# Performance work log

Measured on AMD Instinct MI355X. Metric: run time of the kernel, lower is better.

The kernel has to match this reference:

```python
import jax, jax.numpy as jnp
import numpy as np

B, S, D = 4, 2048, 1024


def setup_inputs() -> dict:
    key = jax.random.key(0)
    ks = jax.random.split(key, 4)
    scale = 1.0 / np.sqrt(D)
    x = jax.random.normal(ks[0], (B, S, D), dtype=jnp.float32)
    Wk = jax.random.normal(ks[1], (D, D), dtype=jnp.float32) * scale
    Wq = jax.random.normal(ks[2], (D, D), dtype=jnp.float32) * scale
    Wv = jax.random.normal(ks[3], (D, D), dtype=jnp.float32) * scale
    bk = jnp.zeros((D,), dtype=jnp.float32)
    bq = jnp.zeros((D,), dtype=jnp.float32)
    bv = jnp.zeros((D,), dtype=jnp.float32)
    return {"x": x, "Wk": Wk, "bk": bk, "Wq": Wq, "bq": bq,
            "Wv": Wv, "bv": bv, "dims": 2}


def correlated_weight(k, q, v, dims):
    # correlation between every query position and every key position,
    # scaled by sqrt(d) for numerical stability (standard correlation attn)
    d = q.shape[-1]
    scores = jnp.einsum("bqd,bkd->bqk", q, k) / jnp.sqrt(jnp.asarray(d, q.dtype))
    w = jax.nn.softmax(scores, axis=dims)          # [B, S, S]
    return jnp.einsum("bqk,bkd->bqd", w, v)        # [B, S, D]


def reference(x, Wk, bk, Wq, bq, Wv, bv, dims):
    # injected key/query/value funcs instantiated as Linear layers
    k = jnp.einsum("bsd,de->bse", x, Wk) + bk
    q = jnp.einsum("bsd,de->bse", x, Wq) + bq
    v = jnp.einsum("bsd,de->bse", x, Wv) + bv
    return correlated_weight(k, q, v, dims)
```

## Files before the change

### kernel.cpp

```cpp
#include <hip/hip_runtime.h>
#include <hip/hip_bf16.h>
#include <stdint.h>


typedef unsigned short u16;
typedef __bf16 bf16x8 __attribute__((ext_vector_type(8)));
typedef float  f32x4  __attribute__((ext_vector_type(4)));
typedef u16    u16x4  __attribute__((ext_vector_type(4)));
typedef u16    u16x8  __attribute__((ext_vector_type(8)));

__device__ __forceinline__ u16 f2bf(float f) {
  union { float f; uint32_t u; } v; v.f = f;
  uint32_t r = v.u + 0x7fffu + ((v.u >> 16) & 1u);
  return (u16)(r >> 16);
}
__device__ __forceinline__ float bf2f(u16 b) {
  union { uint32_t u; float f; } v; v.u = (uint32_t)b << 16; return v.f;
}

#define GLD_LDS16(gp, lp) __builtin_amdgcn_global_load_lds(                   \
    (const __attribute__((address_space(1))) void*)(gp),                      \
    (__attribute__((address_space(3))) void*)(lp), 16, 0, 0)


__global__ __launch_bounds__(256) void conv_x(const float* __restrict__ in,
                                              u16* __restrict__ out, int n) {
  int i = (blockIdx.x * 256 + threadIdx.x) * 4;
  if (i >= n) return;
  float4 v = *(const float4*)(in + i);
  u16x4 o; o.x = f2bf(v.x); o.y = f2bf(v.y); o.z = f2bf(v.z); o.w = f2bf(v.w);
  *(u16x4*)(out + i) = o;
}

__global__ __launch_bounds__(256) void trans_conv_w3(const float* __restrict__ Wq,
                                                     const float* __restrict__ Wk,
                                                     const float* __restrict__ Wv,
                                                     u16* __restrict__ Wt) {
  __shared__ float t[32][33];
  const float* W = blockIdx.z == 0 ? Wq : (blockIdx.z == 1 ? Wk : Wv);
  u16* dst = Wt + (size_t)blockIdx.z * 1024 * 1024;
  int e0 = blockIdx.x * 32, d0 = blockIdx.y * 32;
  #pragma unroll
  for (int i = 0; i < 4; ++i)
    t[threadIdx.y + i * 8][threadIdx.x] =
        W[(size_t)(d0 + threadIdx.y + i * 8) * 1024 + e0 + threadIdx.x];
  __syncthreads();
  #pragma unroll
  for (int i = 0; i < 4; ++i)
    dst[(size_t)(e0 + threadIdx.y + i * 8) * 1024 + d0 + threadIdx.x] =
        f2bf(t[threadIdx.x][threadIdx.y + i * 8]);
}

__global__ __launch_bounds__(256) void concat_bias(const float* __restrict__ bq,
                                                   const float* __restrict__ bk,
                                                   const float* __restrict__ bv,
                                                   float* __restrict__ bc) {
  int i = blockIdx.x * 256 + threadIdx.x;
  if (i >= 3072) return;
  bc[i] = (i < 1024) ? bq[i] : (i < 2048 ? bk[i - 1024] : bv[i - 2048]);
}

__global__ __launch_bounds__(256) void trans_v(const u16* __restrict__ qkv,
                                               u16* __restrict__ vT) {
  __shared__ u16 t[64][72];
  int b = blockIdx.z;
  int s0 = blockIdx.x * 64, e0 = blockIdx.y * 64;
  const u16* src = qkv + (size_t)b * 2048 * 3072 + 2048;
  u16* dst = vT + (size_t)b * 1024 * 2048;
  int tx = threadIdx.x & 7, ty = threadIdx.x >> 3;
  #pragma unroll
  for (int rr = 0; rr < 64; rr += 32)
    *(u16x8*)&t[ty + rr][tx * 8] =
        *(const u16x8*)(src + (size_t)(s0 + ty + rr) * 3072 + e0 + tx * 8);
  __syncthreads();
  #pragma unroll
  for (int rr = 0; rr < 64; rr += 32) {
    int er = ty + rr;
    u16x8 o;
    #pragma unroll
    for (int j = 0; j < 8; ++j) o[j] = t[tx * 8 + j][er];
    *(u16x8*)(dst + (size_t)(e0 + er) * 2048 + s0 + tx * 8) = o;
  }
}


template <int BN, bool OUT_BF16, bool BIAS, bool EXP, bool DIV>
__global__ __launch_bounds__(256)
void gemm16(const u16* __restrict__ A, int lda, long long sA,
            const u16* __restrict__ B, int ldb, long long sB,
            void* __restrict__ C, int ldc, long long sC,
            const float* __restrict__ aux, int K, float scale) {
  constexpr int NJ = BN / 32;
  __shared__ u16 As[128 * 64];
  __shared__ u16 Bs[BN * 64];
  const int lane = threadIdx.x & 63;
  const int wv = threadIdx.x >> 6;

  const u16* Ab = A + (size_t)blockIdx.z * sA + (size_t)blockIdx.y * 128 * lda;
  const u16* Bb = B + (size_t)blockIdx.z * sB + (size_t)blockIdx.x * BN * ldb;

  const int srow = lane >> 3;
  const int scol = ((lane & 7) ^ (lane >> 3)) * 8;
  const int row16 = lane & 15;
  const int quad = lane >> 4;
  const int rx = lane & 7;
  const int wm = (wv >> 1) * 64;
  const int wn = (wv & 1) * (BN / 2);

  f32x4 acc[4][NJ];
  #pragma unroll
  for (int i = 0; i < 4; ++i)
    #pragma unroll
    for (int j = 0; j < NJ; ++j) acc[i][j] = (f32x4)0.0f;

  for (int k0 = 0; k0 < K; k0 += 64) {
    #pragma unroll
    for (int i = 0; i < 4; ++i) {
      int r = wv * 32 + i * 8;
      GLD_LDS16(Ab + (size_t)(r + srow) * lda + k0 + scol, As + r * 64);
    }
    #pragma unroll
    for (int i = 0; i < BN / 32; ++i) {
      int r = wv * (BN / 4) + i * 8;
      GLD_LDS16(Bb + (size_t)(r + srow) * ldb + k0 + scol, Bs + r * 64);
    }
    __syncthreads();

    bf16x8 af[4][2], bfr[NJ][2];
    #pragma unroll
    for (int t = 0; t < 2; ++t) {
      int pc = ((t * 4 + quad) ^ rx) * 8;
      #pragma unroll
      for (int i = 0; i < 4; ++i)
        af[i][t] = *(const bf16x8*)(As + (wm + i * 16 + row16) * 64 + pc);
      #pragma unroll
      for (int j = 0; j < NJ; ++j)
        bfr[j][t] = *(const bf16x8*)(Bs + (wn + j * 16 + row16) * 64 + pc);
    }
    #pragma unroll
    for (int i = 0; i < 4; ++i)
      #pragma unroll
      for (int j = 0; j < NJ; ++j)
        #pragma unroll
        for (int t = 0; t < 2; ++t)
          acc[i][j] = __builtin_amdgcn_mfma_f32_16x16x32_bf16(
              af[i][t], bfr[j][t], acc[i][j], 0, 0, 0);
    __syncthreads();
  }

  const int crow0 = blockIdx.y * 128 + wm + quad * 4;
  const int ccol0 = blockIdx.x * BN + wn + row16;
  u16* Cb = (u16*)C + (size_t)blockIdx.z * sC;
  float* Cf = (float*)C + (size_t)blockIdx.z * sC;
  float rl[4][4];
  if (DIV) {
    const float* lz = aux + (size_t)blockIdx.z * 2048;
    #pragma unroll
    for (int i = 0; i < 4; ++i)
      #pragma unroll
      for (int r = 0; r < 4; ++r)
        rl[i][r] = 1.0f / lz[blockIdx.y * 128 + wm + quad * 4 + i * 16 + r];
  }
  #pragma unroll
  for (int i = 0; i < 4; ++i) {
    #pragma unroll
    for (int r = 0; r < 4; ++r) {
      int m = crow0 + i * 16 + r;
      #pragma unroll
      for (int j = 0; j < NJ; ++j) {
        int n = ccol0 + j * 16;
        float v = acc[i][j][r] * scale;
        if (BIAS) v += aux[n];
        if (EXP) v = exp2f(v);
        if (DIV) v *= rl[i][r];
        if (OUT_BF16) Cb[(size_t)m * ldc + n] = f2bf(v);
        else          Cf[(size_t)m * ldc + n] = v;
      }
    }
  }
}


__global__ __launch_bounds__(256) void rowsum(const u16* __restrict__ P,
                                              float* __restrict__ l) {
  const int lane = threadIdx.x & 63;
  const int row = blockIdx.x * 4 + (threadIdx.x >> 6);
  const u16* r = P + (size_t)row * 2048;
  float s = 0.f;
  #pragma unroll
  for (int c = 0; c < 4; ++c) {
    u16x8 w = *(const u16x8*)(r + c * 512 + lane * 8);
    #pragma unroll
    for (int j = 0; j < 8; ++j) s += bf2f(w[j]);
  }
  #pragma unroll
  for (int off = 32; off > 0; off >>= 1) s += __shfl_down(s, off);
  if (lane == 0) l[row] = s;
}


extern "C" void kernel_launch(void* const* d_in, const int* in_sizes, int n_in,
                              void* d_out, int out_size, void* d_ws, size_t ws_size,
                              hipStream_t stream) {
  const float* x  = (const float*)d_in[0];
  const float* Wk = (const float*)d_in[1];
  const float* bk = (const float*)d_in[2];
  const float* Wq = (const float*)d_in[3];
  const float* bq = (const float*)d_in[4];
  const float* Wv = (const float*)d_in[5];
  const float* bv = (const float*)d_in[6];
  float* out = (float*)d_out;

  char* ws = (char*)d_ws;
  u16*   xb  = (u16*)(ws + 0);
  u16*   wt  = (u16*)(ws + 16777216);
  float* bc  = (float*)(ws + 23068672);
  u16*   qkv = (u16*)(ws + 23080960);
  u16*   vT  = (u16*)(ws + 73412608);
  u16*   P   = (u16*)(ws + 90189824);
  float* l   = (float*)(ws + 123744256);
  (void)in_sizes; (void)n_in; (void)out_size; (void)ws_size;

  conv_x<<<8192, 256, 0, stream>>>(x, xb, 8388608);
  trans_conv_w3<<<dim3(32, 32, 3), dim3(32, 8), 0, stream>>>(Wq, Wk, Wv, wt);
  concat_bias<<<12, 256, 0, stream>>>(bq, bk, bv, bc);

  gemm16<128, true, true, false, false><<<dim3(24, 64, 1), 256, 0, stream>>>(
      xb, 1024, 0LL, wt, 1024, 0LL, (void*)qkv, 3072, 0LL, bc, 1024, 1.0f);

  trans_v<<<dim3(32, 16, 4), 256, 0, stream>>>(qkv, vT);

  gemm16<128, true, false, true, false><<<dim3(16, 16, 4), 256, 0, stream>>>(
      qkv, 3072, 2048LL * 3072, qkv + 1024, 3072, 2048LL * 3072,
      (void*)P, 2048, 2048LL * 2048, nullptr, 1024, 0.03125f * 1.44269504f);

  rowsum<<<2048, 256, 0, stream>>>(P, l);

  gemm16<64, false, false, false, true><<<dim3(16, 16, 4), 256, 0, stream>>>(
      P, 2048, 2048LL * 2048, vT, 2048, 1024LL * 2048,
      out, 1024, 2048LL * 1024, l, 2048, 1.0f);
}
```

Measured before the change: 290.9 us.

## Use 32x32 MFMA, fuse rowsum into exp GEMM via atomics, merge prep kernels

Switches the GEMM inner product from 16x16x32 to 32x32x16 bf16 MFMA tiles, which changes the fragment loads and the epilogue index mapping. The separate rowsum pass is removed: the score GEMM now sums its exp values per row with shuffles and adds them atomically into l. The three input-prep kernels plus the zeroing of l are merged into one launch. This drops a full read of P and two kernel launches, at the cost of atomics and a summation order that is no longer deterministic. The row sums now use the fp32 exp values rather than the rounded bf16 P entries.

```diff
diff --git a/kernel.cpp b/kernel.cpp
--- a/kernel.cpp
+++ b/kernel.cpp
@@ -5,7 +5,7 @@
 
 typedef unsigned short u16;
 typedef __bf16 bf16x8 __attribute__((ext_vector_type(8)));
-typedef float  f32x4  __attribute__((ext_vector_type(4)));
+typedef float  f32x16 __attribute__((ext_vector_type(16)));
 typedef u16    u16x4  __attribute__((ext_vector_type(4)));
 typedef u16    u16x8  __attribute__((ext_vector_type(8)));
 
@@ -14,50 +14,53 @@
   uint32_t r = v.u + 0x7fffu + ((v.u >> 16) & 1u);
   return (u16)(r >> 16);
 }
-__device__ __forceinline__ float bf2f(u16 b) {
-  union { uint32_t u; float f; } v; v.u = (uint32_t)b << 16; return v.f;
-}
 
 #define GLD_LDS16(gp, lp) __builtin_amdgcn_global_load_lds(                   \
     (const __attribute__((address_space(1))) void*)(gp),                      \
     (__attribute__((address_space(3))) void*)(lp), 16, 0, 0)
 
 
-__global__ __launch_bounds__(256) void conv_x(const float* __restrict__ in,
-                                              u16* __restrict__ out, int n) {
-  int i = (blockIdx.x * 256 + threadIdx.x) * 4;
-  if (i >= n) return;
-  float4 v = *(const float4*)(in + i);
-  u16x4 o; o.x = f2bf(v.x); o.y = f2bf(v.y); o.z = f2bf(v.z); o.w = f2bf(v.w);
-  *(u16x4*)(out + i) = o;
-}
-
-__global__ __launch_bounds__(256) void trans_conv_w3(const float* __restrict__ Wq,
-                                                     const float* __restrict__ Wk,
-                                                     const float* __restrict__ Wv,
-                                                     u16* __restrict__ Wt) {
+__global__ __launch_bounds__(256) void prep(const float* __restrict__ x,
+                                            const float* __restrict__ Wq,
+                                            const float* __restrict__ Wk,
+                                            const float* __restrict__ Wv,
+                                            const float* __restrict__ bq,
+                                            const float* __restrict__ bk,
+                                            const float* __restrict__ bv,
+                                            u16* __restrict__ xb,
+                                            u16* __restrict__ wt,
+                                            float* __restrict__ bc,
+                                            float* __restrict__ l) {
   __shared__ float t[32][33];
-  const float* W = blockIdx.z == 0 ? Wq : (blockIdx.z == 1 ? Wk : Wv);
-  u16* dst = Wt + (size_t)blockIdx.z * 1024 * 1024;
-  int e0 = blockIdx.x * 32, d0 = blockIdx.y * 32;
-  #pragma unroll
-  for (int i = 0; i < 4; ++i)
-    t[threadIdx.y + i * 8][threadIdx.x] =
-        W[(size_t)(d0 + threadIdx.y + i * 8) * 1024 + e0 + threadIdx.x];
-  __syncthreads();
-  #pragma unroll
-  for (int i = 0; i < 4; ++i)
-    dst[(size_t)(e0 + threadIdx.y + i * 8) * 1024 + d0 + threadIdx.x] =
-        f2bf(t[threadIdx.x][threadIdx.y + i * 8]);
-}
-
-__global__ __launch_bounds__(256) void concat_bias(const float* __restrict__ bq,
-                                                   const float* __restrict__ bk,
-                                                   const float* __restrict__ bv,
-                                                   float* __restrict__ bc) {
-  int i = blockIdx.x * 256 + threadIdx.x;
-  if (i >= 3072) return;
-  bc[i] = (i < 1024) ? bq[i] : (i < 2048 ? bk[i - 1024] : bv[i - 2048]);
+  const int bid = blockIdx.x;
+  const int tid = threadIdx.x;
+  if (bid < 8192) {
+    int i = (bid * 256 + tid) * 4;
+    float4 v = *(const float4*)(x + i);
+    u16x4 o; o.x = f2bf(v.x); o.y = f2bf(v.y); o.z = f2bf(v.z); o.w = f2bf(v.w);
+    *(u16x4*)(xb + i) = o;
+  } else if (bid < 11264) {
+    int b2 = bid - 8192;
+    int zz = b2 >> 10, rem = b2 & 1023;
+    const float* W = zz == 0 ? Wq : (zz == 1 ? Wk : Wv);
+    u16* dst = wt + (size_t)zz * 1024 * 1024;
+    int e0 = (rem & 31) * 32, d0 = (rem >> 5) * 32;
+    int tx = tid & 31, ty = tid >> 5;
+    #pragma unroll
+    for (int i = 0; i < 4; ++i)
+      t[ty + i * 8][tx] = W[(size_t)(d0 + ty + i * 8) * 1024 + e0 + tx];
+    __syncthreads();
+    #pragma unroll
+    for (int i = 0; i < 4; ++i)
+      dst[(size_t)(e0 + ty + i * 8) * 1024 + d0 + tx] = f2bf(t[tx][ty + i * 8]);
+  } else if (bid < 11276) {
+    int i = (bid - 11264) * 256 + tid;
+    if (i < 3072)
+      bc[i] = (i < 1024) ? bq[i] : (i < 2048 ? bk[i - 1024] : bv[i - 2048]);
+  } else {
+    int i = (bid - 11276) * 256 + tid;
+    l[i] = 0.0f;
+  }
 }
 
 __global__ __launch_bounds__(256) void trans_v(const u16* __restrict__ qkv,
@@ -84,13 +87,14 @@
 }
 
 
-template <int BN, bool OUT_BF16, bool BIAS, bool EXP, bool DIV>
+template <int BN, bool OUT_BF16, bool BIAS, bool EXPSUM, bool DIV>
 __global__ __launch_bounds__(256)
-void gemm16(const u16* __restrict__ A, int lda, long long sA,
-            const u16* __restrict__ B, int ldb, long long sB,
-            void* __restrict__ C, int ldc, long long sC,
-            const float* __restrict__ aux, int K, float scale) {
-  constexpr int NJ = BN / 32;
+void gemm_bt(const u16* __restrict__ A, int lda, long long sA,
+             const u16* __restrict__ B, int ldb, long long sB,
+             void* __restrict__ C, int ldc, long long sC,
+             const float* __restrict__ bias, float* __restrict__ lptr,
+             int K, float scale) {
+  constexpr int NJ = BN / 64;
   __shared__ u16 As[128 * 64];
   __shared__ u16 Bs[BN * 64];
   const int lane = threadIdx.x & 63;
@@ -101,17 +105,17 @@
 
   const int srow = lane >> 3;
   const int scol = ((lane & 7) ^ (lane >> 3)) * 8;
-  const int row16 = lane & 15;
-  const int quad = lane >> 4;
+  const int r32 = lane & 31;
+  const int half = lane >> 5;
   const int rx = lane & 7;
   const int wm = (wv >> 1) * 64;
   const int wn = (wv & 1) * (BN / 2);
 
-  f32x4 acc[4][NJ];
-  #pragma unroll
-  for (int i = 0; i < 4; ++i)
-    #pragma unroll
-    for (int j = 0; j < NJ; ++j) acc[i][j] = (f32x4)0.0f;
+  f32x16 acc[2][NJ];
+  #pragma unroll
+  for (int i = 0; i < 2; ++i)
+    #pragma unroll
+    for (int j = 0; j < NJ; ++j) acc[i][j] = (f32x16)0.0f;
 
   for (int k0 = 0; k0 < K; k0 += 64) {
     #pragma unroll
@@ -126,76 +130,60 @@
     }
     __syncthreads();
 
-    bf16x8 af[4][2], bfr[NJ][2];
-    #pragma unroll
-    for (int t = 0; t < 2; ++t) {
-      int pc = ((t * 4 + quad) ^ rx) * 8;
-      #pragma unroll
-      for (int i = 0; i < 4; ++i)
-        af[i][t] = *(const bf16x8*)(As + (wm + i * 16 + row16) * 64 + pc);
+    bf16x8 af[2][4], bfr[NJ][4];
+    #pragma unroll
+    for (int t = 0; t < 4; ++t) {
+      int pc = ((t * 2 + half) ^ rx) * 8;
+      #pragma unroll
+      for (int i = 0; i < 2; ++i)
+        af[i][t] = *(const bf16x8*)(As + (wm + i * 32 + r32) * 64 + pc);
       #pragma unroll
       for (int j = 0; j < NJ; ++j)
-        bfr[j][t] = *(const bf16x8*)(Bs + (wn + j * 16 + row16) * 64 + pc);
-    }
-    #pragma unroll
-    for (int i = 0; i < 4; ++i)
+        bfr[j][t] = *(const bf16x8*)(Bs + (wn + j * 32 + r32) * 64 + pc);
+    }
+    #pragma unroll
+    for (int i = 0; i < 2; ++i)
       #pragma unroll
       for (int j = 0; j < NJ; ++j)
         #pragma unroll
-        for (int t = 0; t < 2; ++t)
-          acc[i][j] = __builtin_amdgcn_mfma_f32_16x16x32_bf16(
+        for (int t = 0; t < 4; ++t)
+          acc[i][j] = __builtin_amdgcn_mfma_f32_32x32x16_bf16(
               af[i][t], bfr[j][t], acc[i][j], 0, 0, 0);
     __syncthreads();
   }
 
-  const int crow0 = blockIdx.y * 128 + wm + quad * 4;
-  const int ccol0 = blockIdx.x * BN + wn + row16;
+  const int ccol0 = blockIdx.x * BN + wn + r32;
+  const int crow0 = blockIdx.y * 128 + wm + 4 * half;
   u16* Cb = (u16*)C + (size_t)blockIdx.z * sC;
   float* Cf = (float*)C + (size_t)blockIdx.z * sC;
-  float rl[4][4];
-  if (DIV) {
-    const float* lz = aux + (size_t)blockIdx.z * 2048;
-    #pragma unroll
-    for (int i = 0; i < 4; ++i)
-      #pragma unroll
-      for (int r = 0; r < 4; ++r)
-        rl[i][r] = 1.0f / lz[blockIdx.y * 128 + wm + quad * 4 + i * 16 + r];
-  }
-  #pragma unroll
-  for (int i = 0; i < 4; ++i) {
-    #pragma unroll
-    for (int r = 0; r < 4; ++r) {
-      int m = crow0 + i * 16 + r;
+  float* lz = EXPSUM ? (lptr + (size_t)blockIdx.z * 2048) : nullptr;
+  const float* lin = DIV ? (bias + (size_t)blockIdx.z * 2048) : nullptr;
+
+  #pragma unroll
+  for (int i = 0; i < 2; ++i) {
+    #pragma unroll
+    for (int e = 0; e < 16; ++e) {
+      int m = crow0 + i * 32 + (e & 3) + 8 * (e >> 2);
+      float rinv;
+      if (DIV) rinv = 1.0f / lin[m];
+      float rp = 0.f;
       #pragma unroll
       for (int j = 0; j < NJ; ++j) {
-        int n = ccol0 + j * 16;
-        float v = acc[i][j][r] * scale;
-        if (BIAS) v += aux[n];
-        if (EXP) v = exp2f(v);
-        if (DIV) v *= rl[i][r];
+        int n = ccol0 + j * 32;
+        float v = acc[i][j][e] * scale;
+        if (BIAS) v += bias[n];
+        if (EXPSUM) { v = exp2f(v); rp += v; }
+        if (DIV) v *= rinv;
         if (OUT_BF16) Cb[(size_t)m * ldc + n] = f2bf(v);
         else          Cf[(size_t)m * ldc + n] = v;
       }
-    }
-  }
-}
-
-
-__global__ __launch_bounds__(256) void rowsum(const u16* __restrict__ P,
-                                              float* __restrict__ l) {
-  const int lane = threadIdx.x & 63;
-  const int row = blockIdx.x * 4 + (threadIdx.x >> 6);
-  const u16* r = P + (size_t)row * 2048;
-  float s = 0.f;
-  #pragma unroll
-  for (int c = 0; c < 4; ++c) {
-    u16x8 w = *(const u16x8*)(r + c * 512 + lane * 8);
-    #pragma unroll
-    for (int j = 0; j < 8; ++j) s += bf2f(w[j]);
-  }
-  #pragma unroll
-  for (int off = 32; off > 0; off >>= 1) s += __shfl_down(s, off);
-  if (lane == 0) l[row] = s;
+      if (EXPSUM) {
+        #pragma unroll
+        for (int off = 16; off > 0; off >>= 1) rp += __shfl_xor(rp, off);
+        if (r32 == 0) atomicAdd(&lz[m], rp);
+      }
+    }
+  }
 }
 
 
@@ -221,22 +209,21 @@
   float* l   = (float*)(ws + 123744256);
   (void)in_sizes; (void)n_in; (void)out_size; (void)ws_size;
 
-  conv_x<<<8192, 256, 0, stream>>>(x, xb, 8388608);
-  trans_conv_w3<<<dim3(32, 32, 3), dim3(32, 8), 0, stream>>>(Wq, Wk, Wv, wt);
-  concat_bias<<<12, 256, 0, stream>>>(bq, bk, bv, bc);
-
-  gemm16<128, true, true, false, false><<<dim3(24, 64, 1), 256, 0, stream>>>(
-      xb, 1024, 0LL, wt, 1024, 0LL, (void*)qkv, 3072, 0LL, bc, 1024, 1.0f);
+  prep<<<11308, 256, 0, stream>>>(x, Wq, Wk, Wv, bq, bk, bv, xb, wt, bc, l);
+
+  gemm_bt<128, true, true, false, false><<<dim3(24, 64, 1), 256, 0, stream>>>(
+      xb, 1024, 0LL, wt, 1024, 0LL, (void*)qkv, 3072, 0LL, bc, nullptr,
+      1024, 1.0f);
 
   trans_v<<<dim3(32, 16, 4), 256, 0, stream>>>(qkv, vT);
 
-  gemm16<128, true, false, true, false><<<dim3(16, 16, 4), 256, 0, stream>>>(
+  gemm_bt<128, true, false, true, false><<<dim3(16, 16, 4), 256, 0, stream>>>(
       qkv, 3072, 2048LL * 3072, qkv + 1024, 3072, 2048LL * 3072,
-      (void*)P, 2048, 2048LL * 2048, nullptr, 1024, 0.03125f * 1.44269504f);
-
-  rowsum<<<2048, 256, 0, stream>>>(P, l);
-
-  gemm16<64, false, false, false, true><<<dim3(16, 16, 4), 256, 0, stream>>>(
+      (void*)P, 2048, 2048LL * 2048, nullptr, l,
+      1024, 0.03125f * 1.44269504f);
+
+  gemm_bt<64, false, false, false, true><<<dim3(16, 16, 4), 256, 0, stream>>>(
       P, 2048, 2048LL * 2048, vT, 2048, 1024LL * 2048,
-      out, 1024, 2048LL * 1024, l, 2048, 1.0f);
-}
+      out, 1024, 2048LL * 1024, l, nullptr,
+      2048, 1.0f);
+}
```

Result: faster. 283.1 us (-2.7%).
